# Optimization experiments

Hardware: AMD Instinct MI355X
Metric: run time of the kernel (lower is better)

## Reference

```python
import jax, jax.numpy as jnp
import numpy as np

N_HOPS = 3
EDGE_RATE = 0.5   # quirk: floor(rate+u)==1 KEEPS an edge with prob=rate, scaled by 1/(1-rate)
MESS_RATE = 0.1   # standard dropout: zero with prob p, scale kept by 1/(1-p)
N_USERS = 50000
N_ITEMS = 100000
N_NODES = N_USERS + N_ITEMS
NNZ = 1000000
D = 64


def setup_inputs() -> dict:
    key = jax.random.key(0)
    k_u, k_i, k_r, k_c, k_v = jax.random.split(key, 5)
    return {
        "user_embed": jax.random.normal(k_u, (N_USERS, D), dtype=jnp.float32),
        "item_embed": jax.random.normal(k_i, (N_ITEMS, D), dtype=jnp.float32),
        "rows": jax.random.randint(k_r, (NNZ,), 0, N_NODES),
        "cols": jax.random.randint(k_c, (NNZ,), 0, N_NODES),
        "vals": jax.random.uniform(k_v, (NNZ,), dtype=jnp.float32),
    }


def reference(user_embed, item_embed, rows, cols, vals):
    n_users = user_embed.shape[0]
    n_nodes = n_users + item_embed.shape[0]

    all_embed = jnp.concatenate([user_embed, item_embed], axis=0)  # [N, D]
    agg = all_embed
    embs = [all_embed]

    key = jax.random.key(42)
    for hop in range(N_HOPS):
        key, k_e, k_m = jax.random.split(key, 3)
        # edge dropout (faithful to torch._sparse_dropout): keep iff floor(rate+u)==1
        u = jax.random.uniform(k_e, (vals.shape[0],), dtype=vals.dtype)
        keep = (EDGE_RATE + u) >= 1.0
        v = jnp.where(keep, vals, jnp.zeros_like(vals)) * (1.0 / (1.0 - EDGE_RATE))
        # SpMM: out[r] += v * agg[c]  (zeroed edges contribute nothing, same math as
        # rebuilding a smaller sparse tensor, without dynamic shapes)
        msgs = v[:, None] * agg[cols]                       # [nnz, D]
        agg = jax.ops.segment_sum(msgs, rows, num_segments=n_nodes)
        # message dropout (nn.Dropout): zero with prob p, scale kept by 1/(1-p)
        m = jax.random.bernoulli(k_m, 1.0 - MESS_RATE, agg.shape)
        agg = jnp.where(m, agg / (1.0 - MESS_RATE), jnp.zeros_like(agg))
        embs.append(agg)

    embs = jnp.stack(embs, axis=1)  # [N, n_hops+1, D]
    return embs[:n_users], embs[n_users:]
```

## Files before the change

### kernel.cpp

```cpp
#include <hip/hip_runtime.h>
#include <stdint.h>


static constexpr int kUsers = 50000;
static constexpr int kItems = 100000;
static constexpr int kNodes = kUsers + kItems;
static constexpr int kNnz   = 1000000;
static constexpr int kD     = 64;
static constexpr int kHops  = 3;
static constexpr int kRowF  = (kHops + 1) * kD;

static constexpr int kScanBlocks = 147;
static constexpr int kCntN       = kScanBlocks * 1024;

__host__ __device__ inline void tf2x32(uint32_t k0, uint32_t k1,
                                       uint32_t x0, uint32_t x1,
                                       uint32_t &o0, uint32_t &o1) {
  uint32_t ks2 = k0 ^ k1 ^ 0x1BD11BDAu;
  x0 += k0; x1 += k1;
#define TF_R(r) { x0 += x1; x1 = (x1 << (r)) | (x1 >> (32 - (r))); x1 ^= x0; }
  TF_R(13) TF_R(15) TF_R(26) TF_R(6)   x0 += k1;  x1 += ks2 + 1u;
  TF_R(17) TF_R(29) TF_R(16) TF_R(24)  x0 += ks2; x1 += k0 + 2u;
  TF_R(13) TF_R(15) TF_R(26) TF_R(6)   x0 += k0;  x1 += k1 + 3u;
  TF_R(17) TF_R(29) TF_R(16) TF_R(24)  x0 += k1;  x1 += ks2 + 4u;
  TF_R(13) TF_R(15) TF_R(26) TF_R(6)   x0 += ks2; x1 += k0 + 5u;
#undef TF_R
  o0 = x0; o1 = x1;
}

__device__ inline uint32_t jax_bits32(uint32_t k0, uint32_t k1, uint32_t i) {
  uint32_t b1, b2;
  tf2x32(k0, k1, 0u, i, b1, b2);
  return b1 ^ b2;
}

__device__ inline float bits_to_unit(uint32_t b) {
  return __uint_as_float((b >> 9) | 0x3f800000u) - 1.0f;
}


__global__ __launch_bounds__(256) void init_slice0(
    const float4* __restrict__ user, const float4* __restrict__ item,
    float4* __restrict__ out, int4* __restrict__ cnt4) {
  int i = blockIdx.x * 256 + threadIdx.x;
  if (i < kCntN / 4) cnt4[i] = make_int4(0, 0, 0, 0);
  if (i >= kNodes * 16) return;
  int node = i >> 4, q = i & 15;
  float4 v = (node < kUsers) ? user[node * 16 + q]
                             : item[(node - kUsers) * 16 + q];
  out[(size_t)node * (kRowF / 4) + q] = v;
}

__global__ __launch_bounds__(256) void hist_kernel(
    const int* __restrict__ rows, int* __restrict__ cnt) {
  int e = blockIdx.x * 256 + threadIdx.x;
  if (e >= kNnz) return;
  atomicAdd(&cnt[rows[e]], 1);
}

__global__ __launch_bounds__(256) void scanA(
    const int* __restrict__ cnt, int* __restrict__ partials) {
  int t = threadIdx.x;
  int4 v = ((const int4*)(cnt + blockIdx.x * 1024))[t];
  int s = v.x + v.y + v.z + v.w;
  __shared__ int sh[256];
  sh[t] = s; __syncthreads();
  for (int off = 128; off > 0; off >>= 1) {
    if (t < off) sh[t] += sh[t + off];
    __syncthreads();
  }
  if (t == 0) partials[blockIdx.x] = sh[0];
}

__global__ __launch_bounds__(256) void scanB(int* __restrict__ partials) {
  int t = threadIdx.x;
  int v = (t < kScanBlocks) ? partials[t] : 0;
  __shared__ int sh[256];
  sh[t] = v; __syncthreads();
  for (int off = 1; off < 256; off <<= 1) {
    int a = (t >= off) ? sh[t - off] : 0;
    __syncthreads();
    sh[t] += a;
    __syncthreads();
  }
  if (t < kScanBlocks) partials[t] = sh[t] - v;
}

__global__ __launch_bounds__(256) void scanC(
    int* __restrict__ cnt, const int* __restrict__ partials) {
  int t = threadIdx.x;
  int4 v = ((const int4*)(cnt + blockIdx.x * 1024))[t];
  int s = v.x + v.y + v.z + v.w;
  __shared__ int sh[256];
  sh[t] = s; __syncthreads();
  for (int off = 1; off < 256; off <<= 1) {
    int a = (t >= off) ? sh[t - off] : 0;
    __syncthreads();
    sh[t] += a;
    __syncthreads();
  }
  int base = partials[blockIdx.x] + sh[t] - s;
  int4 o;
  o.x = base; o.y = base + v.x; o.z = o.y + v.y; o.w = o.z + v.z;
  ((int4*)(cnt + blockIdx.x * 1024))[t] = o;
}

__global__ __launch_bounds__(256) void scatter_kernel(
    const int* __restrict__ rows, const int* __restrict__ cols,
    const float* __restrict__ vals, int* __restrict__ X,
    uint2* __restrict__ ed,
    uint32_t e00, uint32_t e01, uint32_t e10, uint32_t e11,
    uint32_t e20, uint32_t e21) {
  int e = blockIdx.x * 256 + threadIdx.x;
  if (e >= kNnz) return;
  int r = rows[e];
  int pos = atomicAdd(&X[r], 1);
  float u0 = bits_to_unit(jax_bits32(e00, e01, (uint32_t)e));
  float u1 = bits_to_unit(jax_bits32(e10, e11, (uint32_t)e));
  float u2 = bits_to_unit(jax_bits32(e20, e21, (uint32_t)e));
  uint32_t packed = (uint32_t)cols[e]
                  | ((0.5f + u0 >= 1.0f) ? (1u << 29) : 0u)
                  | ((0.5f + u1 >= 1.0f) ? (1u << 30) : 0u)
                  | ((0.5f + u2 >= 1.0f) ? (1u << 31) : 0u);
  ed[pos] = make_uint2(packed, __float_as_uint(vals[e] * 2.0f));
}

__global__ __launch_bounds__(256) void csr_spmm(
    const int* __restrict__ X, const uint2* __restrict__ ed,
    float* __restrict__ out, int hop, uint32_t km0, uint32_t km1) {
  int pair = blockIdx.x * 4 + (threadIdx.x >> 6);
  int rA = pair * 2;
  if (rA >= kNodes) return;
  int lane = threadIdx.x & 63;
  int g = lane >> 3, q = lane & 7;
  int sA = (rA == 0) ? 0 : X[rA - 1];
  int tA = X[rA];
  int tB = X[rA + 1];
  float uA = bits_to_unit(jax_bits32(km0, km1, (uint32_t)(rA * kD + lane)));
  float uB = bits_to_unit(jax_bits32(km0, km1, (uint32_t)((rA + 1) * kD + lane)));
  float mA = (uA < 0.9f) ? (1.0f / 0.9f) : 0.0f;
  float mB = (uB < 0.9f) ? (1.0f / 0.9f) : 0.0f;
  float4 a0 = make_float4(0.f, 0.f, 0.f, 0.f);
  float4 a1 = make_float4(0.f, 0.f, 0.f, 0.f);
  float4 b0 = make_float4(0.f, 0.f, 0.f, 0.f);
  float4 b1 = make_float4(0.f, 0.f, 0.f, 0.f);
  const float* src = out + (size_t)hop * kD;
  const uint32_t kbit = 1u << (29 + hop);

#define GATHER_FMA(acc0, acc1, rec)                                         \
  {                                                                          \
    float v = __uint_as_float((rec).y);                                      \
    const float* p = src + (size_t)((rec).x & 0x3FFFFu) * kRowF + (q << 3);  \
    float4 x0 = *(const float4*)p;                                           \
    float4 x1 = *(const float4*)(p + 4);                                     \
    acc0.x += v * x0.x; acc0.y += v * x0.y;                                  \
    acc0.z += v * x0.z; acc0.w += v * x0.w;                                  \
    acc1.x += v * x1.x; acc1.y += v * x1.y;                                  \
    acc1.z += v * x1.z; acc1.w += v * x1.w;                                  \
  }

  int iA = sA + g, iB = tA + g;
  while (iA < tA || iB < tB) {
    uint2 eA0, eA1, eB0, eB1;
    const bool hA0 = iA < tA,     hA1 = iA + 8 < tA;
    const bool hB0 = iB < tB,     hB1 = iB + 8 < tB;
    if (hA0) eA0 = ed[iA];
    if (hA1) eA1 = ed[iA + 8];
    if (hB0) eB0 = ed[iB];
    if (hB1) eB1 = ed[iB + 8];
    if (hA0 && (eA0.x & kbit)) GATHER_FMA(a0, a1, eA0);
    if (hA1 && (eA1.x & kbit)) GATHER_FMA(a0, a1, eA1);
    if (hB0 && (eB0.x & kbit)) GATHER_FMA(b0, b1, eB0);
    if (hB1 && (eB1.x & kbit)) GATHER_FMA(b0, b1, eB1);
    iA += 16; iB += 16;
  }
#undef GATHER_FMA

#pragma unroll
  for (int msk = 8; msk <= 32; msk <<= 1) {
    a0.x += __shfl_xor(a0.x, msk); a0.y += __shfl_xor(a0.y, msk);
    a0.z += __shfl_xor(a0.z, msk); a0.w += __shfl_xor(a0.w, msk);
    a1.x += __shfl_xor(a1.x, msk); a1.y += __shfl_xor(a1.y, msk);
    a1.z += __shfl_xor(a1.z, msk); a1.w += __shfl_xor(a1.w, msk);
    b0.x += __shfl_xor(b0.x, msk); b0.y += __shfl_xor(b0.y, msk);
    b0.z += __shfl_xor(b0.z, msk); b0.w += __shfl_xor(b0.w, msk);
    b1.x += __shfl_xor(b1.x, msk); b1.y += __shfl_xor(b1.y, msk);
    b1.z += __shfl_xor(b1.z, msk); b1.w += __shfl_xor(b1.w, msk);
  }
  float w[8];
#pragma unroll
  for (int j = 0; j < 8; ++j) {
    float wA = __shfl(mA, (q << 3) + j);
    float wB = __shfl(mB, (q << 3) + j);
    w[j] = (g == 0) ? wA : wB;
  }
  if (g < 2) {
    int r = rA + g;
    float4 r0, r1;
    if (g == 0) {
      r0 = make_float4(a0.x * w[0], a0.y * w[1], a0.z * w[2], a0.w * w[3]);
      r1 = make_float4(a1.x * w[4], a1.y * w[5], a1.z * w[6], a1.w * w[7]);
    } else {
      r0 = make_float4(b0.x * w[0], b0.y * w[1], b0.z * w[2], b0.w * w[3]);
      r1 = make_float4(b1.x * w[4], b1.y * w[5], b1.z * w[6], b1.w * w[7]);
    }
    float* dst = out + (size_t)r * kRowF + (hop + 1) * kD + (q << 3);
    *(float4*)dst = r0;
    *(float4*)(dst + 4) = r1;
  }
}

__global__ __launch_bounds__(256) void init_full(
    const float4* __restrict__ user, const float4* __restrict__ item,
    float4* __restrict__ out) {
  int i = blockIdx.x * 256 + threadIdx.x;
  if (i >= kNodes * 16) return;
  int node = i >> 4, q = i & 15;
  float4 v = (node < kUsers) ? user[node * 16 + q]
                             : item[(node - kUsers) * 16 + q];
  float4 z = make_float4(0.f, 0.f, 0.f, 0.f);
  float4* row = out + (size_t)node * (kRowF / 4);
  row[q] = v; row[16 + q] = z; row[32 + q] = z; row[48 + q] = z;
}

__global__ __launch_bounds__(256) void spmm_atomic(
    const int* __restrict__ rows, const int* __restrict__ cols,
    const float* __restrict__ vals, float* __restrict__ out, int hop,
    uint32_t k0, uint32_t k1) {
  int e = (int)((blockIdx.x * 256u + threadIdx.x) >> 6);
  if (e >= kNnz) return;
  int lane = threadIdx.x & 63;
  float u = bits_to_unit(jax_bits32(k0, k1, (uint32_t)e));
  if (!(0.5f + u >= 1.0f)) return;
  float v = vals[e] * 2.0f;
  int r = rows[e], c = cols[e];
  float msg = v * out[(size_t)c * kRowF + hop * kD + lane];
  atomicAdd(&out[(size_t)r * kRowF + (hop + 1) * kD + lane], msg);
}

__global__ __launch_bounds__(256) void mdrop_kernel(
    float* __restrict__ out, int hop, uint32_t k0, uint32_t k1) {
  const int total = kNodes * kD;
  int j = blockIdx.x * 256 + threadIdx.x;
  if (j >= total) return;
  float u = bits_to_unit(jax_bits32(k0, k1, (uint32_t)j));
  int node = j >> 6, d = j & 63;
  size_t idx = (size_t)node * kRowF + (hop + 1) * kD + d;
  float a = out[idx];
  out[idx] = (u < 0.9f) ? a / 0.9f : 0.0f;
}

extern "C" void kernel_launch(void* const* d_in, const int* in_sizes, int n_in,
                              void* d_out, int out_size, void* d_ws, size_t ws_size,
                              hipStream_t stream) {
  const float* user = (const float*)d_in[0];
  const float* item = (const float*)d_in[1];
  const int*   rows = (const int*)d_in[2];
  const int*   cols = (const int*)d_in[3];
  const float* vals = (const float*)d_in[4];
  float* out = (float*)d_out;

  uint32_t k0 = 0u, k1 = 42u;
  uint32_t ke[kHops][2], km[kHops][2];
  for (int hop = 0; hop < kHops; ++hop) {
    uint32_t n0, n1;
    tf2x32(k0, k1, 0u, 0u, n0, n1);
    tf2x32(k0, k1, 0u, 1u, ke[hop][0], ke[hop][1]);
    tf2x32(k0, k1, 0u, 2u, km[hop][0], km[hop][1]);
    k0 = n0; k1 = n1;
  }

  const size_t x_b   = (size_t)kCntN * 4;
  const size_t ed_b  = ((size_t)kNnz * 8 + 4095) & ~(size_t)4095;
  const size_t par_b = 4096;
  const size_t need  = x_b + ed_b + par_b;

  if (ws_size >= need) {
    char* ws = (char*)d_ws;
    int*   X        = (int*)ws;
    uint2* ed       = (uint2*)(ws + x_b);
    int*   partials = (int*)(ws + x_b + ed_b);

    init_slice0<<<(kNodes * 16 + 255) / 256, 256, 0, stream>>>(
        (const float4*)user, (const float4*)item, (float4*)out, (int4*)X);
    hist_kernel<<<(kNnz + 255) / 256, 256, 0, stream>>>(rows, X);
    scanA<<<kScanBlocks, 256, 0, stream>>>(X, partials);
    scanB<<<1, 256, 0, stream>>>(partials);
    scanC<<<kScanBlocks, 256, 0, stream>>>(X, partials);
    scatter_kernel<<<(kNnz + 255) / 256, 256, 0, stream>>>(
        rows, cols, vals, X, ed,
        ke[0][0], ke[0][1], ke[1][0], ke[1][1], ke[2][0], ke[2][1]);

    const int nPairs = kNodes / 2;
    for (int hop = 0; hop < kHops; ++hop) {
      csr_spmm<<<(nPairs + 3) / 4, 256, 0, stream>>>(
          X, ed, out, hop, km[hop][0], km[hop][1]);
    }
  } else {
    init_full<<<(kNodes * 16 + 255) / 256, 256, 0, stream>>>(
        (const float4*)user, (const float4*)item, (float4*)out);
    for (int hop = 0; hop < kHops; ++hop) {
      spmm_atomic<<<(kNnz * 64 + 255) / 256, 256, 0, stream>>>(
          rows, cols, vals, out, hop, ke[hop][0], ke[hop][1]);
      mdrop_kernel<<<(kNodes * kD + 255) / 256, 256, 0, stream>>>(
          out, hop, km[hop][0], km[hop][1]);
    }
  }
}
```

Baseline: 303.0 us.

## Gather SpMM inputs from compact fp16 ping-pong embedding buffers

Adds fp16 copies of each hop's embeddings, stored densely (64 halves per node) in two ping-pong workspace buffers. The SpMM gathers from these instead of the strided fp32 output rows, halving the bytes per random gather and improving cache footprint. The edge loop is also simplified from two records per row per iteration to one. This reduces input precision to fp16, which may break numerical tolerance, and adds extra writes of the fp16 copies.

```diff
diff --git a/kernel.cpp b/kernel.cpp
--- a/kernel.cpp
+++ b/kernel.cpp
@@ -1,4 +1,5 @@
 #include <hip/hip_runtime.h>
+#include <hip/hip_fp16.h>
 #include <stdint.h>
 
 
@@ -41,7 +42,8 @@
 
 __global__ __launch_bounds__(256) void init_slice0(
     const float4* __restrict__ user, const float4* __restrict__ item,
-    float4* __restrict__ out, int4* __restrict__ cnt4) {
+    float4* __restrict__ out, __half* __restrict__ plan0,
+    int4* __restrict__ cnt4) {
   int i = blockIdx.x * 256 + threadIdx.x;
   if (i < kCntN / 4) cnt4[i] = make_int4(0, 0, 0, 0);
   if (i >= kNodes * 16) return;
@@ -49,6 +51,12 @@
   float4 v = (node < kUsers) ? user[node * 16 + q]
                              : item[(node - kUsers) * 16 + q];
   out[(size_t)node * (kRowF / 4) + q] = v;
+  if (plan0) {
+    __half2 ha = __floats2half2_rn(v.x, v.y);
+    __half2 hb = __floats2half2_rn(v.z, v.w);
+    uint2 pk = make_uint2(*(uint32_t*)&ha, *(uint32_t*)&hb);
+    *(uint2*)(plan0 + (size_t)node * kD + (q << 2)) = pk;
+  }
 }
 
 __global__ __launch_bounds__(256) void hist_kernel(
@@ -125,9 +133,11 @@
   ed[pos] = make_uint2(packed, __float_as_uint(vals[e] * 2.0f));
 }
 
+template <bool HALF>
 __global__ __launch_bounds__(256) void csr_spmm(
     const int* __restrict__ X, const uint2* __restrict__ ed,
-    float* __restrict__ out, int hop, uint32_t km0, uint32_t km1) {
+    const void* __restrict__ srcv, float* __restrict__ out,
+    __half* __restrict__ dstP, int hop, uint32_t km0, uint32_t km1) {
   int pair = blockIdx.x * 4 + (threadIdx.x >> 6);
   int rA = pair * 2;
   if (rA >= kNodes) return;
@@ -144,35 +154,48 @@
   float4 a1 = make_float4(0.f, 0.f, 0.f, 0.f);
   float4 b0 = make_float4(0.f, 0.f, 0.f, 0.f);
   float4 b1 = make_float4(0.f, 0.f, 0.f, 0.f);
-  const float* src = out + (size_t)hop * kD;
   const uint32_t kbit = 1u << (29 + hop);
 
-#define GATHER_FMA(acc0, acc1, rec)                                         \
+#define GATHER_FMA(acc0, acc1, rec)                                          \
   {                                                                          \
     float v = __uint_as_float((rec).y);                                      \
-    const float* p = src + (size_t)((rec).x & 0x3FFFFu) * kRowF + (q << 3);  \
-    float4 x0 = *(const float4*)p;                                           \
-    float4 x1 = *(const float4*)(p + 4);                                     \
-    acc0.x += v * x0.x; acc0.y += v * x0.y;                                  \
-    acc0.z += v * x0.z; acc0.w += v * x0.w;                                  \
-    acc1.x += v * x1.x; acc1.y += v * x1.y;                                  \
-    acc1.z += v * x1.z; acc1.w += v * x1.w;                                  \
+    uint32_t c = (rec).x & 0x3FFFFu;                                         \
+    if (HALF) {                                                              \
+      const __half* src = (const __half*)srcv;                               \
+      float4 raw = *(const float4*)(src + (size_t)c * kD + (q << 3));        \
+      const __half2* h2 = (const __half2*)&raw;                              \
+      float2 f0 = __half22float2(h2[0]);                                     \
+      float2 f1 = __half22float2(h2[1]);                                     \
+      float2 f2 = __half22float2(h2[2]);                                     \
+      float2 f3 = __half22float2(h2[3]);                                     \
+      acc0.x += v * f0.x; acc0.y += v * f0.y;                                \
+      acc0.z += v * f1.x; acc0.w += v * f1.y;                                \
+      acc1.x += v * f2.x; acc1.y += v * f2.y;                                \
+      acc1.z += v * f3.x; acc1.w += v * f3.y;                                \
+    } else {                                                                 \
+      const float* src = (const float*)srcv;                                 \
+      const float* p = src + (size_t)c * kRowF + (q << 3);                   \
+      float4 x0 = *(const float4*)p;                                         \
+      float4 x1 = *(const float4*)(p + 4);                                   \
+      acc0.x += v * x0.x; acc0.y += v * x0.y;                                \
+      acc0.z += v * x0.z; acc0.w += v * x0.w;                                \
+      acc1.x += v * x1.x; acc1.y += v * x1.y;                                \
+      acc1.z += v * x1.z; acc1.w += v * x1.w;                                \
+    }                                                                        \
   }
 
   int iA = sA + g, iB = tA + g;
   while (iA < tA || iB < tB) {
-    uint2 eA0, eA1, eB0, eB1;
-    const bool hA0 = iA < tA,     hA1 = iA + 8 < tA;
-    const bool hB0 = iB < tB,     hB1 = iB + 8 < tB;
-    if (hA0) eA0 = ed[iA];
-    if (hA1) eA1 = ed[iA + 8];
-    if (hB0) eB0 = ed[iB];
-    if (hB1) eB1 = ed[iB + 8];
-    if (hA0 && (eA0.x & kbit)) GATHER_FMA(a0, a1, eA0);
-    if (hA1 && (eA1.x & kbit)) GATHER_FMA(a0, a1, eA1);
-    if (hB0 && (eB0.x & kbit)) GATHER_FMA(b0, b1, eB0);
-    if (hB1 && (eB1.x & kbit)) GATHER_FMA(b0, b1, eB1);
-    iA += 16; iB += 16;
+    if (iA < tA) {
+      uint2 m = ed[iA];
+      if (m.x & kbit) GATHER_FMA(a0, a1, m);
+      iA += 8;
+    }
+    if (iB < tB) {
+      uint2 m = ed[iB];
+      if (m.x & kbit) GATHER_FMA(b0, b1, m);
+      iB += 8;
+    }
   }
 #undef GATHER_FMA
 
@@ -207,6 +230,18 @@
     float* dst = out + (size_t)r * kRowF + (hop + 1) * kD + (q << 3);
     *(float4*)dst = r0;
     *(float4*)(dst + 4) = r1;
+    if (HALF && dstP) {
+      __half2 h0 = __floats2half2_rn(r0.x, r0.y);
+      __half2 h1 = __floats2half2_rn(r0.z, r0.w);
+      __half2 h2 = __floats2half2_rn(r1.x, r1.y);
+      __half2 h3 = __floats2half2_rn(r1.z, r1.w);
+      float4 pk;
+      ((uint32_t*)&pk)[0] = *(uint32_t*)&h0;
+      ((uint32_t*)&pk)[1] = *(uint32_t*)&h1;
+      ((uint32_t*)&pk)[2] = *(uint32_t*)&h2;
+      ((uint32_t*)&pk)[3] = *(uint32_t*)&h3;
+      *(float4*)(dstP + (size_t)r * kD + (q << 3)) = pk;
+    }
   }
 }
 
@@ -270,19 +305,25 @@
     k0 = n0; k1 = n1;
   }
 
-  const size_t x_b   = (size_t)kCntN * 4;
-  const size_t ed_b  = ((size_t)kNnz * 8 + 4095) & ~(size_t)4095;
-  const size_t par_b = 4096;
-  const size_t need  = x_b + ed_b + par_b;
-
-  if (ws_size >= need) {
+  const size_t x_b    = (size_t)kCntN * 4;
+  const size_t ed_b   = ((size_t)kNnz * 8 + 4095) & ~(size_t)4095;
+  const size_t plan_b = (size_t)kNodes * kD * 2;
+  const size_t par_b  = 4096;
+  const size_t needB  = x_b + ed_b + par_b;
+  const size_t needA  = x_b + ed_b + 2 * plan_b + par_b;
+
+  if (ws_size >= needB) {
+    const bool halfPath = (ws_size >= needA);
     char* ws = (char*)d_ws;
-    int*   X        = (int*)ws;
-    uint2* ed       = (uint2*)(ws + x_b);
-    int*   partials = (int*)(ws + x_b + ed_b);
+    int*    X        = (int*)ws;
+    uint2*  ed       = (uint2*)(ws + x_b);
+    __half* planA    = halfPath ? (__half*)(ws + x_b + ed_b) : nullptr;
+    __half* planB    = halfPath ? (__half*)(ws + x_b + ed_b + plan_b) : nullptr;
+    int*    partials = (int*)(ws + (halfPath ? needA : needB) - par_b);
 
     init_slice0<<<(kNodes * 16 + 255) / 256, 256, 0, stream>>>(
-        (const float4*)user, (const float4*)item, (float4*)out, (int4*)X);
+        (const float4*)user, (const float4*)item, (float4*)out, planA,
+        (int4*)X);
     hist_kernel<<<(kNnz + 255) / 256, 256, 0, stream>>>(rows, X);
     scanA<<<kScanBlocks, 256, 0, stream>>>(X, partials);
     scanB<<<1, 256, 0, stream>>>(partials);
@@ -292,9 +333,19 @@
         ke[0][0], ke[0][1], ke[1][0], ke[1][1], ke[2][0], ke[2][1]);
 
     const int nPairs = kNodes / 2;
+    const int grid   = (nPairs + 3) / 4;
     for (int hop = 0; hop < kHops; ++hop) {
-      csr_spmm<<<(nPairs + 3) / 4, 256, 0, stream>>>(
-          X, ed, out, hop, km[hop][0], km[hop][1]);
+      if (halfPath) {
+        const __half* src = (hop & 1) ? planB : planA;
+        __half* dstP = (hop == kHops - 1) ? nullptr
+                                          : ((hop & 1) ? planA : planB);
+        csr_spmm<true><<<grid, 256, 0, stream>>>(
+            X, ed, (const void*)src, out, dstP, hop, km[hop][0], km[hop][1]);
+      } else {
+        csr_spmm<false><<<grid, 256, 0, stream>>>(
+            X, ed, (const void*)(out + (size_t)hop * kD), out, nullptr,
+            hop, km[hop][0], km[hop][1]);
+      }
     }
   } else {
     init_full<<<(kNodes * 16 + 255) / 256, 256, 0, stream>>>(
```

Result: slower. 311.4 us (+2.7%).
